# Kernel tuning notes

Measured on AMD Instinct MI355X. Metric: run time of the kernel, lower is better.

Reference implementation:

```python
import jax, jax.numpy as jnp
import numpy as np

DIM = 128
HEADS = 4
SCALE = (DIM / HEADS) ** -0.5


def setup_inputs() -> dict:
    key = jax.random.key(0)
    k1, k2, k3, k4, k5 = jax.random.split(key, 5)
    B, J = 8192, 81
    return {
        "Q": jax.random.normal(k1, (B, 1, DIM), dtype=jnp.float32),
        "K": jax.random.normal(k2, (B, J, DIM), dtype=jnp.float32),
        "V": jax.random.normal(k3, (B, J, DIM), dtype=jnp.float32),
        "Q_r": jax.random.normal(k4, (B, J, DIM), dtype=jnp.float32),
        "K_r": jax.random.normal(k5, (B, J, DIM), dtype=jnp.float32),
    }


def _split_heads(x):
    # [b, n, heads*d] -> [b, heads, n, d]
    b, n, _ = x.shape
    return x.reshape(b, n, HEADS, DIM // HEADS).transpose(0, 2, 1, 3)


def reference(Q, K, V, Q_r, K_r):
    Qh = _split_heads(Q)      # [b, h, 1, d]
    Kh = _split_heads(K)      # [b, h, j, d]
    Vh = _split_heads(V)      # [b, h, j, d]
    Qrh = _split_heads(Q_r)   # [b, h, j, d]
    Krh = _split_heads(K_r)   # [b, h, j, d]

    # content-content and content-position scores: [b, h, 1, j]
    c_c = jnp.einsum('bhid,bhjd->bhij', Qh, Kh) * SCALE
    c_p = jnp.einsum('bhid,bhjd->bhij', Qh, Krh) * SCALE
    # position-content: rowwise dot of Q_r and K (the original's expand/squeeze
    # trick reduces to a per-j dot product), broadcast over the i=1 axis
    p_c = (jnp.sum(Qrh * Kh, axis=-1) * SCALE)[:, :, None, :]  # [b, h, 1, j]

    attn = jax.nn.softmax(c_c + c_p + p_c, axis=-1)            # [b, h, 1, j]
    out = jnp.einsum('bhij,bhjd->bhid', attn, Vh)              # [b, h, 1, d]
    b = Q.shape[0]
    return out.transpose(0, 2, 1, 3).reshape(b, 1, DIM)
```

## Files before the change

kernel.cpp:

```cpp
#include <hip/hip_runtime.h>
#include <math.h>

#define J_LEN 81
#define DIM 128
#define HEADS 4
#define HD 32
#define SCALE 0.17677669529663687f

__global__ __launch_bounds__(256) void mhar_kernel(
    const float* __restrict__ Q,
    const float* __restrict__ K,
    const float* __restrict__ V,
    const float* __restrict__ Qr,
    const float* __restrict__ Kr,
    float* __restrict__ out)
{
    const int b = blockIdx.x;
    const int t = threadIdx.x;

    __shared__ float  s_q[DIM];
    __shared__ float  s_sc[HEADS][88];
    __shared__ float4 s_red[8][32];

    if (t < DIM) s_q[t] = Q[(size_t)b * DIM + t];
    __syncthreads();

    const int wave = t >> 6;
    const int lane = t & 63;
    const int g    = lane >> 3;
    const int sub  = lane & 7;

    const float4* K4  = (const float4*)K;
    const float4* Kr4 = (const float4*)Kr;
    const float4* Qr4 = (const float4*)Qr;
    const float4* V4  = (const float4*)V;

    {
        const int h = wave;
        float4 q4 = ((const float4*)s_q)[h * 8 + sub];
        for (int jt = 0; jt < 11; ++jt) {
            int j = jt * 8 + g;
            if (j < J_LEN) {
                size_t idx = ((size_t)b * J_LEN + j) * 32 + h * 8 + sub;
                float4 k  = K4[idx];
                float4 kr = Kr4[idx];
                float4 qr = Qr4[idx];
                float partial =
                      q4.x * (k.x + kr.x) + qr.x * k.x
                    + q4.y * (k.y + kr.y) + qr.y * k.y
                    + q4.z * (k.z + kr.z) + qr.z * k.z
                    + q4.w * (k.w + kr.w) + qr.w * k.w;
                partial += __shfl_xor(partial, 1);
                partial += __shfl_xor(partial, 2);
                partial += __shfl_xor(partial, 4);
                if (sub == 0) s_sc[h][j] = partial * SCALE;
            }
        }
    }
    __syncthreads();

    {
        float s0 = (lane < J_LEN)      ? s_sc[wave][lane]      : -INFINITY;
        float s1 = (lane + 64 < J_LEN) ? s_sc[wave][lane + 64] : -INFINITY;
        float m = fmaxf(s0, s1);
        #pragma unroll
        for (int off = 32; off > 0; off >>= 1)
            m = fmaxf(m, __shfl_xor(m, off));
        float e0 = (lane < J_LEN)      ? __expf(s0 - m) : 0.f;
        float e1 = (lane + 64 < J_LEN) ? __expf(s1 - m) : 0.f;
        float sum = e0 + e1;
        #pragma unroll
        for (int off = 32; off > 0; off >>= 1)
            sum += __shfl_xor(sum, off);
        float inv = 1.f / sum;
        if (lane < J_LEN)      s_sc[wave][lane]      = e0 * inv;
        if (lane + 64 < J_LEN) s_sc[wave][lane + 64] = e1 * inv;
    }
    __syncthreads();

    {
        const int j_off = t >> 5;
        const int d4    = t & 31;
        const int h2    = d4 >> 3;
        float4 acc = {0.f, 0.f, 0.f, 0.f};
        for (int jt = 0; jt < 11; ++jt) {
            int j = jt * 8 + j_off;
            if (j < J_LEN) {
                float  p = s_sc[h2][j];
                float4 v = V4[((size_t)b * J_LEN + j) * 32 + d4];
                acc.x += p * v.x;
                acc.y += p * v.y;
                acc.z += p * v.z;
                acc.w += p * v.w;
            }
        }
        s_red[j_off][d4] = acc;
    }
    __syncthreads();

    if (t < 32) {
        float4 r = s_red[0][t];
        #pragma unroll
        for (int i = 1; i < 8; ++i) {
            float4 a = s_red[i][t];
            r.x += a.x; r.y += a.y; r.z += a.z; r.w += a.w;
        }
        ((float4*)out)[(size_t)b * 32 + t] = r;
    }
}

extern "C" void kernel_launch(void* const* d_in, const int* in_sizes, int n_in,
                              void* d_out, int out_size, void* d_ws, size_t ws_size,
                              hipStream_t stream) {
    const float* Q  = (const float*)d_in[0];
    const float* K  = (const float*)d_in[1];
    const float* V  = (const float*)d_in[2];
    const float* Qr = (const float*)d_in[3];
    const float* Kr = (const float*)d_in[4];
    float* out = (float*)d_out;
    const int B = in_sizes[0] / DIM;
    mhar_kernel<<<B, 256, 0, stream>>>(Q, K, V, Qr, Kr, out);
}
```

Before: 996.8 us.

## Map one wavefront per batch row and drop block-wide barriers

Each 64-lane wavefront now handles one whole batch element, and each block covers four batch elements. Each wave streams two J rows per iteration across all four heads and does the softmax for all heads itself. The final cross-lane sum is a single shuffle instead of a shared-memory reduction, so the __syncthreads barriers are replaced by compiler memory fences within the wave. The aim is to remove barrier stalls and shared-memory traffic. The cost is that each wave runs a longer serial loop with fewer loads in flight per iteration, and rows past J are handled with clamped redundant loads.

```diff
diff --git a/kernel.cpp b/kernel.cpp
--- a/kernel.cpp
+++ b/kernel.cpp
@@ -3,8 +3,6 @@
 
 #define J_LEN 81
 #define DIM 128
-#define HEADS 4
-#define HD 32
 #define SCALE 0.17677669529663687f
 
 __global__ __launch_bounds__(256) void mhar_kernel(
@@ -13,100 +11,86 @@
     const float* __restrict__ V,
     const float* __restrict__ Qr,
     const float* __restrict__ Kr,
-    float* __restrict__ out)
+    float* __restrict__ out,
+    int B)
 {
-    const int b = blockIdx.x;
-    const int t = threadIdx.x;
-
-    __shared__ float  s_q[DIM];
-    __shared__ float  s_sc[HEADS][88];
-    __shared__ float4 s_red[8][32];
-
-    if (t < DIM) s_q[t] = Q[(size_t)b * DIM + t];
-    __syncthreads();
-
+    const int t    = threadIdx.x;
     const int wave = t >> 6;
     const int lane = t & 63;
-    const int g    = lane >> 3;
-    const int sub  = lane & 7;
+    const int b    = blockIdx.x * 4 + wave;
+    if (b >= B) return;
+
+    const int rsub = lane >> 5;
+    const int c    = lane & 31;
+    const int h    = c >> 3;
+    const int sub  = c & 7;
+
+    __shared__ float s_sc[4][4][88];
+    float (*sc)[88] = s_sc[wave];
 
     const float4* K4  = (const float4*)K;
     const float4* Kr4 = (const float4*)Kr;
     const float4* Qr4 = (const float4*)Qr;
     const float4* V4  = (const float4*)V;
 
-    {
-        const int h = wave;
-        float4 q4 = ((const float4*)s_q)[h * 8 + sub];
-        for (int jt = 0; jt < 11; ++jt) {
-            int j = jt * 8 + g;
-            if (j < J_LEN) {
-                size_t idx = ((size_t)b * J_LEN + j) * 32 + h * 8 + sub;
-                float4 k  = K4[idx];
-                float4 kr = Kr4[idx];
-                float4 qr = Qr4[idx];
-                float partial =
-                      q4.x * (k.x + kr.x) + qr.x * k.x
-                    + q4.y * (k.y + kr.y) + qr.y * k.y
-                    + q4.z * (k.z + kr.z) + qr.z * k.z
-                    + q4.w * (k.w + kr.w) + qr.w * k.w;
-                partial += __shfl_xor(partial, 1);
-                partial += __shfl_xor(partial, 2);
-                partial += __shfl_xor(partial, 4);
-                if (sub == 0) s_sc[h][j] = partial * SCALE;
-            }
-        }
+    const size_t rowbase = (size_t)b * J_LEN;
+    const float4 q4 = ((const float4*)Q)[(size_t)b * 32 + c];
+
+    for (int jt = 0; jt < 41; ++jt) {
+        const int j  = jt * 2 + rsub;
+        const int jc = (j < J_LEN) ? j : (J_LEN - 1);
+        const size_t idx = (rowbase + jc) * 32 + c;
+        float4 k  = K4[idx];
+        float4 kr = Kr4[idx];
+        float4 qr = Qr4[idx];
+        float p = q4.x * (k.x + kr.x) + qr.x * k.x
+                + q4.y * (k.y + kr.y) + qr.y * k.y
+                + q4.z * (k.z + kr.z) + qr.z * k.z
+                + q4.w * (k.w + kr.w) + qr.w * k.w;
+        p += __shfl_xor(p, 1);
+        p += __shfl_xor(p, 2);
+        p += __shfl_xor(p, 4);
+        if (sub == 0 && j < J_LEN) sc[h][j] = p * SCALE;
     }
-    __syncthreads();
+    asm volatile("" ::: "memory");
 
-    {
-        float s0 = (lane < J_LEN)      ? s_sc[wave][lane]      : -INFINITY;
-        float s1 = (lane + 64 < J_LEN) ? s_sc[wave][lane + 64] : -INFINITY;
+    #pragma unroll
+    for (int hh = 0; hh < 4; ++hh) {
+        float s0 = sc[hh][lane];
+        float s1 = (lane + 64 < J_LEN) ? sc[hh][lane + 64] : -INFINITY;
         float m = fmaxf(s0, s1);
         #pragma unroll
         for (int off = 32; off > 0; off >>= 1)
             m = fmaxf(m, __shfl_xor(m, off));
-        float e0 = (lane < J_LEN)      ? __expf(s0 - m) : 0.f;
+        float e0 = __expf(s0 - m);
         float e1 = (lane + 64 < J_LEN) ? __expf(s1 - m) : 0.f;
         float sum = e0 + e1;
         #pragma unroll
         for (int off = 32; off > 0; off >>= 1)
             sum += __shfl_xor(sum, off);
-        float inv = 1.f / sum;
-        if (lane < J_LEN)      s_sc[wave][lane]      = e0 * inv;
-        if (lane + 64 < J_LEN) s_sc[wave][lane + 64] = e1 * inv;
+        const float inv = 1.f / sum;
+        sc[hh][lane] = e0 * inv;
+        if (lane + 64 < 88) sc[hh][lane + 64] = e1 * inv;
     }
-    __syncthreads();
+    asm volatile("" ::: "memory");
 
-    {
-        const int j_off = t >> 5;
-        const int d4    = t & 31;
-        const int h2    = d4 >> 3;
-        float4 acc = {0.f, 0.f, 0.f, 0.f};
-        for (int jt = 0; jt < 11; ++jt) {
-            int j = jt * 8 + j_off;
-            if (j < J_LEN) {
-                float  p = s_sc[h2][j];
-                float4 v = V4[((size_t)b * J_LEN + j) * 32 + d4];
-                acc.x += p * v.x;
-                acc.y += p * v.y;
-                acc.z += p * v.z;
-                acc.w += p * v.w;
-            }
-        }
-        s_red[j_off][d4] = acc;
+    float4 acc = {0.f, 0.f, 0.f, 0.f};
+    for (int jt = 0; jt < 41; ++jt) {
+        const int j  = jt * 2 + rsub;
+        const int jc = (j < J_LEN) ? j : (J_LEN - 1);
+        const float pw = sc[h][j];
+        float4 v = V4[(rowbase + jc) * 32 + c];
+        acc.x += pw * v.x;
+        acc.y += pw * v.y;
+        acc.z += pw * v.z;
+        acc.w += pw * v.w;
     }
-    __syncthreads();
-
-    if (t < 32) {
-        float4 r = s_red[0][t];
-        #pragma unroll
-        for (int i = 1; i < 8; ++i) {
-            float4 a = s_red[i][t];
-            r.x += a.x; r.y += a.y; r.z += a.z; r.w += a.w;
-        }
-        ((float4*)out)[(size_t)b * 32 + t] = r;
-    }
+    acc.x += __shfl_xor(acc.x, 32);
+    acc.y += __shfl_xor(acc.y, 32);
+    acc.z += __shfl_xor(acc.z, 32);
+    acc.w += __shfl_xor(acc.w, 32);
+    if (lane < 32)
+        ((float4*)out)[(size_t)b * 32 + c] = acc;
 }
 
 extern "C" void kernel_launch(void* const* d_in, const int* in_sizes, int n_in,
@@ -119,5 +103,6 @@
     const float* Kr = (const float*)d_in[4];
     float* out = (float*)d_out;
     const int B = in_sizes[0] / DIM;
-    mhar_kernel<<<B, 256, 0, stream>>>(Q, K, V, Qr, Kr, out);
+    const int grid = (B + 3) / 4;
+    mhar_kernel<<<grid, 256, 0, stream>>>(Q, K, V, Qr, Kr, out, B);
 }
```

After: 1.022 ms. 2.5% more time.
